# Kernel optimization log

Measured on AMD Instinct MI355X. Metric: run time of the kernel, lower is better.

Reference implementation:

```python
import jax, jax.numpy as jnp
import numpy as np

ACT_FACTOR = 1.0

def high_order_act(A, params):
    # A: [B, G, K] (K = arity), params: [G, 2**K, D]
    A_ind = jnp.argsort(A, axis=2)                      # [B, G, K]
    A_sort = jnp.take_along_axis(A, A_ind, axis=2)      # [B, G, K]
    coef = jnp.concatenate([A_sort[:, :, :1], A_sort[:, :, 1:] - A_sort[:, :, :-1]], axis=2)
    # reversed cumulative sum of 2**A_ind along K
    pw = (2 ** A_ind).astype(jnp.int32)
    params_A_ind = jnp.flip(jnp.cumsum(jnp.flip(pw, axis=2), axis=2), axis=2)  # [B, G, K]
    G = params.shape[0]
    g_idx = jnp.arange(G)[None, :, None]                # [1, G, 1]
    params_gather = params[g_idx, params_A_ind, :]      # [B, G, K, D]
    # torch einsum 'jikl,ijk->ijl' with params_gather laid out [G,B,K,D];
    # here layout is [B,G,K,D], same contraction over K:
    return jnp.einsum('bgkd,bgk->bgd', params_gather, coef)

def setup_inputs() -> dict:
    key = jax.random.key(0)
    k1, k2 = jax.random.split(key)
    B, G, K, D = 4096, 512, 4, 8
    X = jax.random.normal(k1, (B, G * K), dtype=jnp.float32)
    params = jax.random.uniform(k2, (G, 2 ** K, D), dtype=jnp.float32) / ACT_FACTOR
    return {"X": X, "params": params}

def reference(X, params):
    B = X.shape[0]
    G, _, D = params.shape
    K = X.shape[1] // G
    X1 = X.reshape(B, G, K)
    out1 = high_order_act(X1, params) * ACT_FACTOR   # [B, G, D]
    return out1.reshape(B, G * D)
```

## Files before the change

### kernel.cpp

```cpp
#include <hip/hip_runtime.h>


#define BB 4096
#define GG 512
#define G_TILE 16
#define NB 8
#define G_STRIDE 33

typedef float f32x4 __attribute__((ext_vector_type(4)));

__global__ __launch_bounds__(256) void monoact_kernel(
    const float4* __restrict__ X4,
    const float4* __restrict__ P4,
    float4* __restrict__ O4)
{
    __shared__ float4 lds_p[G_TILE * G_STRIDE];

    const int tid = threadIdx.x;
    const int g0 = blockIdx.x * G_TILE;
    const int b0 = blockIdx.y * (8 * NB);

    for (int j = tid; j < G_TILE * 32; j += 256) {
        const int g_l = j >> 5;
        const int rem = j & 31;
        const int h_s = rem >> 4;
        const int r_s = rem & 15;
        lds_p[g_l * G_STRIDE + rem] = P4[(g0 + g_l) * 32 + r_s * 2 + h_s];
    }
    __syncthreads();

    const int gh  = tid & 31;
    const int g_l = gh >> 1;
    const int h   = gh & 1;
    const int b_l = tid >> 5;
    const int g = g0 + g_l;
    const float4* __restrict__ pg = lds_p + g_l * G_STRIDE + h * 16;

    const float4 aTop = pg[15];

    float4 xr[NB];
#pragma unroll
    for (int it = 0; it < NB; ++it) {
        xr[it] = X4[(b0 + it * 8 + b_l) * 512 + g];
    }

#pragma unroll
    for (int it = 0; it < NB; ++it) {
        const int b = b0 + it * 8 + b_l;
        const float4 x = xr[it];

        float v[4] = {x.x, x.y, x.z, x.w};
        int   id[4] = {0, 1, 2, 3};
#define CSWAP(a, c)                                               \
        {                                                         \
            bool sw = v[a] > v[c];                                \
            float tv = sw ? v[a] : v[c];                          \
            v[a] = sw ? v[c] : v[a];                              \
            v[c] = tv;                                            \
            int ti = sw ? id[a] : id[c];                          \
            id[a] = sw ? id[c] : id[a];                           \
            id[c] = ti;                                           \
        }
        CSWAP(0, 1)
        CSWAP(2, 3)
        CSWAP(0, 2)
        CSWAP(1, 3)
        CSWAP(1, 2)
#undef CSWAP

        const float c0 = v[0];
        const float c1 = v[1] - v[0];
        const float c2 = v[2] - v[1];
        const float c3 = v[3] - v[2];

        const int r1 = 15 - (1 << id[0]);
        const int r2 = r1 - (1 << id[1]);
        const int r3 = 1 << id[3];

        const float4 a1 = pg[r1];
        const float4 a2 = pg[r2];
        const float4 a3 = pg[r3];

        float4 o;
        o.x = fmaf(c0, aTop.x, fmaf(c1, a1.x, fmaf(c2, a2.x, c3 * a3.x)));
        o.y = fmaf(c0, aTop.y, fmaf(c1, a1.y, fmaf(c2, a2.y, c3 * a3.y)));
        o.z = fmaf(c0, aTop.z, fmaf(c1, a1.z, fmaf(c2, a2.z, c3 * a3.z)));
        o.w = fmaf(c0, aTop.w, fmaf(c1, a1.w, fmaf(c2, a2.w, c3 * a3.w)));

        __builtin_nontemporal_store(*(const f32x4*)&o,
                                    (f32x4*)&O4[b * 1024 + g0 * 2 + gh]);
    }
}

extern "C" void kernel_launch(void* const* d_in, const int* in_sizes, int n_in,
                              void* d_out, int out_size, void* d_ws, size_t ws_size,
                              hipStream_t stream) {
    const float4* X4 = (const float4*)d_in[0];
    const float4* P4 = (const float4*)d_in[1];
    float4* O4 = (float4*)d_out;

    dim3 grid(GG / G_TILE, BB / (8 * NB));
    monoact_kernel<<<grid, 256, 0, stream>>>(X4, P4, O4);
}
```

Before: 92.99 us.

## Store params in LDS as fp16 and compute full 8-wide output per thread

Parameters are converted to half precision when staged in shared memory, so a single 16-byte LDS read yields all 8 output channels. Each thread now handles one group across all D instead of half of it, and the top row is loaded from global memory in fp32. The block covers 16 rows per iteration with NB reduced to 4, which keeps the grid size unchanged. The aim is to halve LDS traffic per output, at the cost of fp16 rounding error in three of the four gathered terms and half-warp-strided output stores.

```diff
diff --git a/kernel.cpp b/kernel.cpp
--- a/kernel.cpp
+++ b/kernel.cpp
@@ -4,52 +4,57 @@
 #define BB 4096
 #define GG 512
 #define G_TILE 16
-#define NB 8
-#define G_STRIDE 33
+#define NB 4
+#define R_STRIDE 17
 
-typedef float f32x4 __attribute__((ext_vector_type(4)));
+typedef _Float16 h16x8 __attribute__((ext_vector_type(8)));
+typedef float    f32x4 __attribute__((ext_vector_type(4)));
 
 __global__ __launch_bounds__(256) void monoact_kernel(
     const float4* __restrict__ X4,
     const float4* __restrict__ P4,
     float4* __restrict__ O4)
 {
-    __shared__ float4 lds_p[G_TILE * G_STRIDE];
+    __shared__ h16x8 lds_p[G_TILE * R_STRIDE];
 
     const int tid = threadIdx.x;
     const int g0 = blockIdx.x * G_TILE;
-    const int b0 = blockIdx.y * (8 * NB);
+    const int b0 = blockIdx.y * (16 * NB);
 
-    for (int j = tid; j < G_TILE * 32; j += 256) {
-        const int g_l = j >> 5;
-        const int rem = j & 31;
-        const int h_s = rem >> 4;
-        const int r_s = rem & 15;
-        lds_p[g_l * G_STRIDE + rem] = P4[(g0 + g_l) * 32 + r_s * 2 + h_s];
+    {
+        const int g_s = tid >> 4;
+        const int r_s = tid & 15;
+        const float4 plo = P4[(g0 + g_s) * 32 + r_s * 2 + 0];
+        const float4 phi = P4[(g0 + g_s) * 32 + r_s * 2 + 1];
+        h16x8 hv;
+        hv[0] = (_Float16)plo.x; hv[1] = (_Float16)plo.y;
+        hv[2] = (_Float16)plo.z; hv[3] = (_Float16)plo.w;
+        hv[4] = (_Float16)phi.x; hv[5] = (_Float16)phi.y;
+        hv[6] = (_Float16)phi.z; hv[7] = (_Float16)phi.w;
+        lds_p[g_s * R_STRIDE + r_s] = hv;
     }
+
+    const int g_l = tid & 15;
+    const int b_l = tid >> 4;
+    const int g   = g0 + g_l;
+    const h16x8* __restrict__ pg = lds_p + g_l * R_STRIDE;
+
+    const float4 t0 = P4[g * 32 + 30];
+    const float4 t1 = P4[g * 32 + 31];
+
     __syncthreads();
-
-    const int gh  = tid & 31;
-    const int g_l = gh >> 1;
-    const int h   = gh & 1;
-    const int b_l = tid >> 5;
-    const int g = g0 + g_l;
-    const float4* __restrict__ pg = lds_p + g_l * G_STRIDE + h * 16;
-
-    const float4 aTop = pg[15];
 
     float4 xr[NB];
 #pragma unroll
-    for (int it = 0; it < NB; ++it) {
-        xr[it] = X4[(b0 + it * 8 + b_l) * 512 + g];
-    }
+    for (int it = 0; it < NB; ++it)
+        xr[it] = X4[(size_t)(b0 + it * 16 + b_l) * 512 + g];
 
 #pragma unroll
     for (int it = 0; it < NB; ++it) {
-        const int b = b0 + it * 8 + b_l;
+        const int b = b0 + it * 16 + b_l;
         const float4 x = xr[it];
 
-        float v[4] = {x.x, x.y, x.z, x.w};
+        float v[4]  = {x.x, x.y, x.z, x.w};
         int   id[4] = {0, 1, 2, 3};
 #define CSWAP(a, c)                                               \
         {                                                         \
@@ -77,18 +82,23 @@
         const int r2 = r1 - (1 << id[1]);
         const int r3 = 1 << id[3];
 
-        const float4 a1 = pg[r1];
-        const float4 a2 = pg[r2];
-        const float4 a3 = pg[r3];
+        const h16x8 a1 = pg[r1];
+        const h16x8 a2 = pg[r2];
+        const h16x8 a3 = pg[r3];
 
-        float4 o;
-        o.x = fmaf(c0, aTop.x, fmaf(c1, a1.x, fmaf(c2, a2.x, c3 * a3.x)));
-        o.y = fmaf(c0, aTop.y, fmaf(c1, a1.y, fmaf(c2, a2.y, c3 * a3.y)));
-        o.z = fmaf(c0, aTop.z, fmaf(c1, a1.z, fmaf(c2, a2.z, c3 * a3.z)));
-        o.w = fmaf(c0, aTop.w, fmaf(c1, a1.w, fmaf(c2, a2.w, c3 * a3.w)));
+        float o[8];
+#pragma unroll
+        for (int d = 0; d < 8; ++d) {
+            const float base = (d < 4) ? (&t0.x)[d] : (&t1.x)[d - 4];
+            o[d] = fmaf(c0, base,
+                   fmaf(c1, (float)a1[d],
+                   fmaf(c2, (float)a2[d], c3 * (float)a3[d])));
+        }
 
-        __builtin_nontemporal_store(*(const f32x4*)&o,
-                                    (f32x4*)&O4[b * 1024 + g0 * 2 + gh]);
+        f32x4 olo = {o[0], o[1], o[2], o[3]};
+        f32x4 ohi = {o[4], o[5], o[6], o[7]};
+        __builtin_nontemporal_store(olo, (f32x4*)&O4[(size_t)b * 1024 + g * 2 + 0]);
+        __builtin_nontemporal_store(ohi, (f32x4*)&O4[(size_t)b * 1024 + g * 2 + 1]);
     }
 }
 
@@ -99,6 +109,6 @@
     const float4* P4 = (const float4*)d_in[1];
     float4* O4 = (float4*)d_out;
 
-    dim3 grid(GG / G_TILE, BB / (8 * NB));
+    dim3 grid(GG / G_TILE, BB / (16 * NB));
     monoact_kernel<<<grid, 256, 0, stream>>>(X4, P4, O4);
 }
```

Result: slower. 100.5 us (+8.0%).
